# Kernel optimization log

Hardware: AMD Instinct MI355X
Metric: run time of the kernel (lower is better)

## Reference

```python
import jax, jax.numpy as jnp
import numpy as np

EMBED_DIM = 1024
NUM_HEADS = 16
HEAD_DIM = EMBED_DIM // NUM_HEADS
FEATURE_EPS = 1e-06
DEN_EPS = 1e-06


def setup_inputs() -> dict:
    key = jax.random.key(0)
    k_x, k_qw, k_qb, k_ow, k_ob = jax.random.split(key, 5)
    b, l = 2, 2048
    x = jax.random.normal(k_x, (b, l, EMBED_DIM), dtype=jnp.float32)
    s = 1.0 / np.sqrt(EMBED_DIM)
    qkv_w = jax.random.uniform(k_qw, (3 * EMBED_DIM, EMBED_DIM), minval=-s, maxval=s, dtype=jnp.float32)
    qkv_b = jax.random.uniform(k_qb, (3 * EMBED_DIM,), minval=-s, maxval=s, dtype=jnp.float32)
    out_w = jax.random.uniform(k_ow, (EMBED_DIM, EMBED_DIM), minval=-s, maxval=s, dtype=jnp.float32)
    out_b = jax.random.uniform(k_ob, (EMBED_DIM,), minval=-s, maxval=s, dtype=jnp.float32)
    return {"x": x, "qkv_w": qkv_w, "qkv_b": qkv_b, "out_w": out_w, "out_b": out_b}


def reference(x, qkv_w, qkv_b, out_w, out_b):
    b, l, e = x.shape
    # qkv projection -> (3, b, h, l, d)
    qkv = (x @ qkv_w.T + qkv_b).reshape(b, l, 3, NUM_HEADS, HEAD_DIM)
    qkv = jnp.transpose(qkv, (2, 0, 3, 1, 4))
    q, k, v = qkv[0], qkv[1], qkv[2]
    # phi(x) = relu(x) + eps
    q = jax.nn.relu(q) + FEATURE_EPS
    k = jax.nn.relu(k) + FEATURE_EPS
    # running outer-product state: (b, h, l, d, d)
    kv = jnp.cumsum(jnp.einsum('bhld,bhle->bhlde', k, v), axis=2)
    k_cum = jnp.cumsum(k, axis=2)
    num = jnp.einsum('bhld,bhlde->bhle', q, kv)
    den = jnp.maximum(jnp.einsum('bhld,bhld->bhl', q, k_cum)[..., None], DEN_EPS)
    out = num / den  # (b, h, l, d)
    out = jnp.transpose(out, (0, 2, 1, 3)).reshape(b, l, e)
    return out @ out_w.T + out_b
```

## Files before the change

kernel.cpp:

```cpp
#include <hip/hip_runtime.h>
#include <hip/hip_bf16.h>
#include <cstdint>

#define B_ 2
#define L_ 2048
#define E_ 1024
#define H_ 16
#define D_ 64
#define N3_ 3072
#define NCHUNK 32
#define CHUNK 64

typedef __attribute__((ext_vector_type(8))) short bf16x8;
typedef __attribute__((ext_vector_type(4))) float f32x4;

__device__ __forceinline__ unsigned short f2bf(float f) {
  unsigned u = __float_as_uint(f);
  unsigned r = (u + 0x7fffu + ((u >> 16) & 1u)) >> 16;
  return (unsigned short)r;
}

__global__ __launch_bounds__(256) void k_cvt_all(
    const float* __restrict__ x, const float* __restrict__ qkv_w,
    const float* __restrict__ out_w, unsigned short* __restrict__ xb,
    unsigned short* __restrict__ wqkv, unsigned short* __restrict__ wout) {
  const int i = blockIdx.x * 256 + threadIdx.x;
  const float* src;
  unsigned short* dst;
  int j;
  if (i < 1048576)      { src = x;     dst = xb;   j = i; }
  else if (i < 1835008) { src = qkv_w; dst = wqkv; j = i - 1048576; }
  else                  { src = out_w; dst = wout; j = i - 1835008; }
  float4 v = reinterpret_cast<const float4*>(src)[j];
  ushort4 o;
  o.x = f2bf(v.x); o.y = f2bf(v.y); o.z = f2bf(v.z); o.w = f2bf(v.w);
  reinterpret_cast<ushort4*>(dst)[j] = o;
}

__global__ __launch_bounds__(512, 2) void k_gemm256_qkv(
    const unsigned short* __restrict__ A,
    const unsigned short* __restrict__ Bm,
    const float* __restrict__ bias,
    unsigned short* __restrict__ Qb, unsigned short* __restrict__ Kb,
    unsigned short* __restrict__ Vb) {
  __shared__ short As[2][256 * 64];
  __shared__ short Bs[2][192 * 64];
  const int tid = threadIdx.x;
  const int lane = tid & 63, wave = tid >> 6;
  const int wm = wave >> 2, wn = wave & 3;
  const int bid0 = blockIdx.y * 16 + blockIdx.x;
  const int bid = (bid0 & 7) * 32 + (bid0 >> 3);
  const int m0 = (bid >> 4) * 256, n0 = (bid & 15) * 192;
  const int srow = tid >> 3, scol = (tid & 7) * 8;
  const int ssw = (srow & 7) * 8;
  const int l15 = lane & 15, l16 = lane >> 4;
  const int sw = (l15 & 7) * 8;
  const int NT = 16;

  f32x4 acc[8][3];
#pragma unroll
  for (int i = 0; i < 8; ++i)
#pragma unroll
    for (int j = 0; j < 3; ++j) acc[i][j] = (f32x4){0.f, 0.f, 0.f, 0.f};

  auto stageA = [&](int d, int kt) {
#pragma unroll
    for (int i = 0; i < 4; ++i) {
      const int r = i * 64 + srow;
      const unsigned short* src = &A[(size_t)(m0 + r) * 1024 + kt * 64 + (scol ^ ssw)];
      __builtin_amdgcn_global_load_lds(
          (const __attribute__((address_space(1))) unsigned int*)src,
          (__attribute__((address_space(3))) unsigned int*)&As[d][r * 64 + scol], 16, 0, 0);
    }
  };
  auto stageB = [&](int d, int kt) {
#pragma unroll
    for (int i = 0; i < 3; ++i) {
      const int r = i * 64 + srow;
      const unsigned short* src = &Bm[(size_t)(n0 + r) * 1024 + kt * 64 + (scol ^ ssw)];
      __builtin_amdgcn_global_load_lds(
          (const __attribute__((address_space(1))) unsigned int*)src,
          (__attribute__((address_space(3))) unsigned int*)&Bs[d][r * 64 + scol], 16, 0, 0);
    }
  };
  auto lda = [&](bf16x8 (&dv)[8], int d, int kh) {
#pragma unroll
    for (int mi = 0; mi < 8; ++mi) {
      const int r = wm * 128 + mi * 16 + l15;
      dv[mi] = *reinterpret_cast<const bf16x8*>(&As[d][r * 64 + ((l16 * 8 + kh * 32) ^ sw)]);
    }
  };
  auto ldb = [&](bf16x8 (&dv)[3], int d, int kh) {
#pragma unroll
    for (int ni = 0; ni < 3; ++ni) {
      const int r = wn * 48 + ni * 16 + l15;
      dv[ni] = *reinterpret_cast<const bf16x8*>(&Bs[d][r * 64 + ((l16 * 8 + kh * 32) ^ sw)]);
    }
  };
  auto quad = [&](const bf16x8 (&af)[8], const bf16x8 (&bf)[3], int nb, int ne) {
    __builtin_amdgcn_s_setprio(1);
#pragma unroll
    for (int mi = 0; mi < 8; ++mi)
      for (int nn = nb; nn < ne; ++nn)
        acc[mi][nn] = __builtin_amdgcn_mfma_f32_16x16x32_bf16(af[mi], bf[nn], acc[mi][nn], 0, 0, 0);
    __builtin_amdgcn_s_setprio(0);
  };

  stageA(0, 0); stageB(0, 0); stageA(1, 1);
  asm volatile("s_waitcnt vmcnt(4)" ::: "memory");
  __builtin_amdgcn_s_barrier();

  bf16x8 af0[8], af1[8], bf0[3], bf1[3];
  for (int t = 0; t < NT; ++t) {
    const int d = t & 1;
    lda(af0, d, 0); ldb(bf0, d, 0);
    if (t + 1 < NT) stageB(d ^ 1, t + 1);
    __builtin_amdgcn_s_barrier();
    asm volatile("s_waitcnt lgkmcnt(0)" ::: "memory");
    __builtin_amdgcn_sched_barrier(0);
    quad(af0, bf0, 0, 2);
    __builtin_amdgcn_s_barrier();
    lda(af1, d, 1); ldb(bf1, d, 1);
    __builtin_amdgcn_s_barrier();
    asm volatile("s_waitcnt lgkmcnt(0)" ::: "memory");
    __builtin_amdgcn_sched_barrier(0);
    quad(af0, bf0, 2, 3);
    __builtin_amdgcn_s_barrier();
    if (t + 2 < NT) stageA(d, t + 2);
    quad(af1, bf1, 0, 2);
    __builtin_amdgcn_s_barrier();
    quad(af1, bf1, 2, 3);
    if (t + 2 < NT) asm volatile("s_waitcnt vmcnt(4)" ::: "memory");
    else            asm volatile("s_waitcnt vmcnt(0)" ::: "memory");
    __builtin_amdgcn_s_barrier();
  }

#pragma unroll
  for (int mi = 0; mi < 8; ++mi) {
#pragma unroll
    for (int ni = 0; ni < 3; ++ni) {
      const int col = n0 + wn * 48 + ni * 16 + l15;
      const float bv = bias[col];
      const int t = col >> 10, hd = col & 1023;
      const int h = hd >> 6, dd = hd & 63;
#pragma unroll
      for (int j = 0; j < 4; ++j) {
        const int row = m0 + wm * 128 + mi * 16 + l16 * 4 + j;
        const float val = acc[mi][ni][j] + bv;
        const int b = row >> 11, l = row & 2047;
        const size_t dst = (((size_t)(b * 16 + h)) * 2048 + l) * 64 + dd;
        if (t == 0)      Qb[dst] = f2bf(fmaxf(val, 0.f) + 1e-6f);
        else if (t == 1) Kb[dst] = f2bf(fmaxf(val, 0.f) + 1e-6f);
        else             Vb[dst] = f2bf(val);
      }
    }
  }
}

__global__ __launch_bounds__(256) void k_gemm_out(
    const unsigned short* __restrict__ A, const unsigned short* __restrict__ Bm,
    const float* __restrict__ bias, float* __restrict__ O, const int K) {
  __shared__ short As[128 * 32];
  __shared__ short Bs[128 * 32];
  const int tid = threadIdx.x;
  const int lane = tid & 63;
  const int wave = tid >> 6;
  const int wr = wave >> 1, wc = wave & 1;
  const int m0 = blockIdx.y * 128, n0 = blockIdx.x * 128;
  const int srow = tid >> 2;
  const int scol = (tid & 3) << 3;
  f32x4 acc[4][4];
#pragma unroll
  for (int i = 0; i < 4; ++i)
#pragma unroll
    for (int j = 0; j < 4; ++j) acc[i][j] = (f32x4){0.f, 0.f, 0.f, 0.f};

  const int l15 = lane & 15, l16 = lane >> 4;
  const int aoff0 = (wr * 64 + l15) * 32 + l16 * 8;
  const int boff0 = (wc * 64 + l15) * 32 + l16 * 8;

  for (int k0 = 0; k0 < K; k0 += 32) {
    const short* gA = (const short*)&A[(size_t)(m0 + srow) * K + k0 + scol];
    const short* gB = (const short*)&Bm[(size_t)(n0 + srow) * K + k0 + scol];
    __builtin_amdgcn_global_load_lds(
        (const __attribute__((address_space(1))) unsigned int*)gA,
        (__attribute__((address_space(3))) unsigned int*)&As[tid * 8], 16, 0, 0);
    __builtin_amdgcn_global_load_lds(
        (const __attribute__((address_space(1))) unsigned int*)(gA + (size_t)64 * K),
        (__attribute__((address_space(3))) unsigned int*)&As[2048 + tid * 8], 16, 0, 0);
    __builtin_amdgcn_global_load_lds(
        (const __attribute__((address_space(1))) unsigned int*)gB,
        (__attribute__((address_space(3))) unsigned int*)&Bs[tid * 8], 16, 0, 0);
    __builtin_amdgcn_global_load_lds(
        (const __attribute__((address_space(1))) unsigned int*)(gB + (size_t)64 * K),
        (__attribute__((address_space(3))) unsigned int*)&Bs[2048 + tid * 8], 16, 0, 0);
    __syncthreads();
    bf16x8 af[4], bfr[4];
#pragma unroll
    for (int f = 0; f < 4; ++f)
      af[f] = *reinterpret_cast<const bf16x8*>(&As[aoff0 + f * 16 * 32]);
#pragma unroll
    for (int f = 0; f < 4; ++f)
      bfr[f] = *reinterpret_cast<const bf16x8*>(&Bs[boff0 + f * 16 * 32]);
#pragma unroll
    for (int m = 0; m < 4; ++m)
#pragma unroll
      for (int n = 0; n < 4; ++n)
        acc[m][n] = __builtin_amdgcn_mfma_f32_16x16x32_bf16(af[m], bfr[n], acc[m][n], 0, 0, 0);
    __syncthreads();
  }

  const int rbase = l16 * 4;
#pragma unroll
  for (int m = 0; m < 4; ++m) {
#pragma unroll
    for (int n = 0; n < 4; ++n) {
      const int col = n0 + wc * 64 + n * 16 + l15;
      const float bv = bias[col];
#pragma unroll
      for (int j = 0; j < 4; ++j) {
        const int row = m0 + wr * 64 + m * 16 + rbase + j;
        O[(size_t)row * 1024 + col] = acc[m][n][j] + bv;
      }
    }
  }
}

__global__ __launch_bounds__(128) void k_chunkB(
    const unsigned short* __restrict__ Kb, const unsigned short* __restrict__ Vb,
    float* __restrict__ ST, unsigned short* __restrict__ Vtb) {
  __shared__ __align__(16) unsigned short Kt[64 * 72];
  __shared__ __align__(16) unsigned short Vt[64 * 72];
  const int tid = threadIdx.x;
  const int lane = tid & 63, w = tid >> 6;
  const int c = lane & 15, g = lane >> 4;
  const int bid = blockIdx.x;
  const int bh = bid >> 5, ch = bid & 31;
  const size_t base = ((size_t)bh * L_ + (size_t)ch * CHUNK) * D_;
  const int l = tid >> 1, hf = tid & 1;
  bf16x8 kv[4], vv[4];
#pragma unroll
  for (int i = 0; i < 4; ++i) {
    kv[i] = *reinterpret_cast<const bf16x8*>(&Kb[base + (size_t)l * 64 + hf * 32 + i * 8]);
    vv[i] = *reinterpret_cast<const bf16x8*>(&Vb[base + (size_t)l * 64 + hf * 32 + i * 8]);
  }
#pragma unroll
  for (int i = 0; i < 4; ++i)
#pragma unroll
    for (int r = 0; r < 8; ++r) {
      const int d = hf * 32 + i * 8 + r;
      Kt[d * 72 + l] = (unsigned short)kv[i][r];
      Vt[d * 72 + l] = (unsigned short)vv[i][r];
    }
  __syncthreads();
  bf16x8 kf[4][2], vf[2][2];
#pragma unroll
  for (int dt = 0; dt < 4; ++dt)
#pragma unroll
    for (int kh = 0; kh < 2; ++kh)
      kf[dt][kh] = *reinterpret_cast<const bf16x8*>(&Kt[(dt * 16 + c) * 72 + g * 8 + kh * 32]);
#pragma unroll
  for (int ei = 0; ei < 2; ++ei)
#pragma unroll
    for (int kh = 0; kh < 2; ++kh)
      vf[ei][kh] = *reinterpret_cast<const bf16x8*>(&Vt[((w * 2 + ei) * 16 + c) * 72 + g * 8 + kh * 32]);
  f32x4 acc[2][4];
#pragma unroll
  for (int ei = 0; ei < 2; ++ei)
#pragma unroll
    for (int dt = 0; dt < 4; ++dt) acc[ei][dt] = (f32x4){0.f, 0.f, 0.f, 0.f};
#pragma unroll
  for (int ei = 0; ei < 2; ++ei)
#pragma unroll
    for (int dt = 0; dt < 4; ++dt)
#pragma unroll
      for (int kh = 0; kh < 2; ++kh)
        acc[ei][dt] = __builtin_amdgcn_mfma_f32_16x16x32_bf16(vf[ei][kh], kf[dt][kh], acc[ei][dt], 0, 0, 0);
  const size_t stbase = (size_t)bid * 5120;
#pragma unroll
  for (int ei = 0; ei < 2; ++ei)
#pragma unroll
    for (int dt = 0; dt < 4; ++dt)
#pragma unroll
      for (int r = 0; r < 4; ++r)
        ST[stbase + (size_t)((w * 2 + ei) * 16 + 4 * g + r) * 64 + dt * 16 + c] = acc[ei][dt][r];
#pragma unroll
  for (int ei = 0; ei < 2; ++ei)
#pragma unroll
    for (int kh = 0; kh < 2; ++kh)
      *reinterpret_cast<bf16x8*>(&Vtb[(size_t)bid * 4096 + ((w * 2 + ei) * 16 + c) * 64 + g * 8 + kh * 32]) = vf[ei][kh];
  if (w == 0) {
    const short one = (c == 0) ? (short)0x3F80 : (short)0;
    bf16x8 of;
#pragma unroll
    for (int r = 0; r < 8; ++r) of[r] = one;
    f32x4 az[4];
#pragma unroll
    for (int dt = 0; dt < 4; ++dt) az[dt] = (f32x4){0.f, 0.f, 0.f, 0.f};
#pragma unroll
    for (int dt = 0; dt < 4; ++dt)
#pragma unroll
      for (int kh = 0; kh < 2; ++kh)
        az[dt] = __builtin_amdgcn_mfma_f32_16x16x32_bf16(of, kf[dt][kh], az[dt], 0, 0, 0);
    if (g == 0) {
#pragma unroll
      for (int dt = 0; dt < 4; ++dt)
        ST[stbase + 64 * 64 + dt * 16 + c] = az[dt][0];
    }
  }
}

__global__ __launch_bounds__(256) void k_prefix2(const float* __restrict__ ST,
                                                 unsigned short* __restrict__ STb) {
  const int bh = blockIdx.x;
  const int e = blockIdx.y * 256 + threadIdx.x;
  if (e >= 4160) return;
  const size_t base = (size_t)bh * NCHUNK * 5120 + e;
  float run = 0.f;
  for (int cc = 0; cc < NCHUNK; ++cc) {
    const float t = ST[base + (size_t)cc * 5120];
    STb[base + (size_t)cc * 5120] = f2bf(run);
    run += t;
  }
}

__global__ __launch_bounds__(256) void k_chunkD(
    const unsigned short* __restrict__ Qb, const unsigned short* __restrict__ Kb,
    const unsigned short* __restrict__ Vtb, const unsigned short* __restrict__ STb,
    unsigned short* __restrict__ attnb) {
  __shared__ __align__(16) unsigned short P[4][1024];
  const int tid = threadIdx.x;
  const int lane = tid & 63, lt = tid >> 6;
  const int c = lane & 15, g = lane >> 4;
  const int bid = blockIdx.x;
  const int bh = bid >> 5, ch = bid & 31;
  const int b = bh >> 4, h = bh & 15;
  const size_t qkbase = ((size_t)bh * L_ + (size_t)ch * CHUNK) * D_;
  bf16x8 q[2], k4[4][2], s[5][2], vt[4][2], pa[2];
#pragma unroll
  for (int kh = 0; kh < 2; ++kh)
    q[kh] = *reinterpret_cast<const bf16x8*>(&Qb[qkbase + (size_t)(lt * 16 + c) * 64 + g * 8 + kh * 32]);
#pragma unroll
  for (int jt = 0; jt < 4; ++jt)
#pragma unroll
    for (int kh = 0; kh < 2; ++kh)
      k4[jt][kh] = *reinterpret_cast<const bf16x8*>(&Kb[qkbase + (size_t)(jt * 16 + c) * 64 + g * 8 + kh * 32]);
  const size_t stbase = (size_t)bid * 5120;
#pragma unroll
  for (int et = 0; et < 5; ++et)
#pragma unroll
    for (int kh = 0; kh < 2; ++kh)
      s[et][kh] = *reinterpret_cast<const bf16x8*>(&STb[stbase + (size_t)(et * 16 + c) * 64 + g * 8 + kh * 32]);
#pragma unroll
  for (int et = 0; et < 4; ++et)
#pragma unroll
    for (int kh = 0; kh < 2; ++kh)
      vt[et][kh] = *reinterpret_cast<const bf16x8*>(&Vtb[(size_t)bid * 4096 + (size_t)(et * 16 + c) * 64 + g * 8 + kh * 32]);

  char* Pb = (char*)&P[lt][0];
  const int swz = (c & 7) << 4;
#pragma unroll
  for (int jt = 0; jt < 4; ++jt) {
    unsigned pk0 = 0, pk1 = 0;
    if (jt <= lt) {
      f32x4 a1 = (f32x4){0.f, 0.f, 0.f, 0.f};
#pragma unroll
      for (int kh = 0; kh < 2; ++kh)
        a1 = __builtin_amdgcn_mfma_f32_16x16x32_bf16(k4[jt][kh], q[kh], a1, 0, 0, 0);
      if (jt == lt) {
#pragma unroll
        for (int r = 0; r < 4; ++r) a1[r] = (4 * g + r <= c) ? a1[r] : 0.f;
      }
      pk0 = (unsigned)f2bf(a1[0]) | ((unsigned)f2bf(a1[1]) << 16);
      pk1 = (unsigned)f2bf(a1[2]) | ((unsigned)f2bf(a1[3]) << 16);
    }
    *reinterpret_cast<unsigned*>(Pb + ((c * 128 + 32 * jt + 8 * g + 0) ^ swz)) = pk0;
    *reinterpret_cast<unsigned*>(Pb + ((c * 128 + 32 * jt + 8 * g + 4) ^ swz)) = pk1;
  }
#pragma unroll
  for (int kh = 0; kh < 2; ++kh)
    pa[kh] = *reinterpret_cast<const bf16x8*>(Pb + (c * 128 + ((16 * g + 64 * kh) ^ swz)));

  f32x4 acc2[5];
#pragma unroll
  for (int et = 0; et < 5; ++et) acc2[et] = (f32x4){0.f, 0.f, 0.f, 0.f};
  const short one = (c == 0) ? (short)0x3F80 : (short)0;
  bf16x8 of;
#pragma unroll
  for (int r = 0; r < 8; ++r) of[r] = one;
#pragma unroll
  for (int et = 0; et < 5; ++et) {
#pragma unroll
    for (int kh = 0; kh < 2; ++kh) {
      acc2[et] = __builtin_amdgcn_mfma_f32_16x16x32_bf16(q[kh], s[et][kh], acc2[et], 0, 0, 0);
      bf16x8 vv = (et < 4) ? vt[et][kh] : of;
      acc2[et] = __builtin_amdgcn_mfma_f32_16x16x32_bf16(pa[kh], vv, acc2[et], 0, 0, 0);
    }
  }
  float inv[4];
#pragma unroll
  for (int r = 0; r < 4; ++r) {
    float dv = __shfl(acc2[4][r], lane & 48, 64);
    inv[r] = 1.f / fmaxf(dv, 1e-6f);
  }
  const size_t obase = ((size_t)b * L_ + (size_t)ch * CHUNK + (size_t)lt * 16) * E_ + (size_t)h * 64;
#pragma unroll
  for (int et = 0; et < 4; ++et)
#pragma unroll
    for (int r = 0; r < 4; ++r)
      attnb[obase + (size_t)(4 * g + r) * E_ + et * 16 + c] = f2bf(acc2[et][r] * inv[r]);
}

extern "C" void kernel_launch(void* const* d_in, const int* in_sizes, int n_in,
                              void* d_out, int out_size, void* d_ws, size_t ws_size,
                              hipStream_t stream) {
  const float* x = (const float*)d_in[0];
  const float* qkv_w = (const float*)d_in[1];
  const float* qkv_b = (const float*)d_in[2];
  const float* out_w = (const float*)d_in[3];
  const float* out_b = (const float*)d_in[4];
  float* out = (float*)d_out;

  const size_t SZ = (size_t)B_ * H_ * L_ * D_;
  char* p = (char*)d_ws;
  unsigned short* Qb = (unsigned short*)p;    p += SZ * 2;
  unsigned short* Kb = (unsigned short*)p;    p += SZ * 2;
  unsigned short* Vb = (unsigned short*)p;    p += SZ * 2;
  unsigned short* Vtb = (unsigned short*)p;   p += (size_t)1024 * 4096 * 2;
  float* ST = (float*)p;                      p += (size_t)1024 * 5120 * 4;
  unsigned short* STb = (unsigned short*)p;   p += (size_t)1024 * 5120 * 2;
  unsigned short* xb = (unsigned short*)p;    p += SZ * 2;
  unsigned short* wqkv = (unsigned short*)p;  p += (size_t)N3_ * E_ * 2;
  unsigned short* wout = (unsigned short*)p;  p += (size_t)E_ * E_ * 2;
  unsigned short* attnb = (unsigned short*)p; p += SZ * 2;

  dim3 blk(256);
  k_cvt_all<<<dim3(8192), blk, 0, stream>>>(x, qkv_w, out_w, xb, wqkv, wout);
  k_gemm256_qkv<<<dim3(16, 16), dim3(512), 0, stream>>>(xb, wqkv, qkv_b, Qb, Kb, Vb);
  k_chunkB<<<dim3(1024), dim3(128), 0, stream>>>(Kb, Vb, ST, Vtb);
  k_prefix2<<<dim3(32, 17), blk, 0, stream>>>(ST, STb);
  k_chunkD<<<dim3(1024), blk, 0, stream>>>(Qb, Kb, Vtb, STb, attnb);
  k_gemm_out<<<dim3(E_ / 128, (B_ * L_) / 128), blk, 0, stream>>>(
      attnb, wout, out_b, out, E_);
}
```

Baseline: 173.6 us.

## Pipeline output GEMM with 256x64 double-buffered tiles and store chunk states in bf16

Replaces the single-buffered 128x128 output projection GEMM with a 512-thread kernel that uses 256x64 tiles. It double-buffers shared memory with asynchronous global-to-LDS loads, XOR-swizzles the LDS layout, remaps blocks for locality and raises wave priority around MFMA groups. The goal is to overlap loads with compute and cut LDS bank conflicts. It also stores per-chunk states in bf16 instead of fp32, halving traffic between chunkB and the prefix kernel, at the cost of extra rounding before the prefix sum.

```diff
diff --git a/kernel.cpp b/kernel.cpp
--- a/kernel.cpp
+++ b/kernel.cpp
@@ -18,6 +18,9 @@
   unsigned u = __float_as_uint(f);
   unsigned r = (u + 0x7fffu + ((u >> 16) & 1u)) >> 16;
   return (unsigned short)r;
+}
+__device__ __forceinline__ float bf2f(unsigned short u) {
+  return __uint_as_float(((unsigned)u) << 16);
 }
 
 __global__ __launch_bounds__(256) void k_cvt_all(
@@ -157,78 +160,107 @@
   }
 }
 
-__global__ __launch_bounds__(256) void k_gemm_out(
-    const unsigned short* __restrict__ A, const unsigned short* __restrict__ Bm,
-    const float* __restrict__ bias, float* __restrict__ O, const int K) {
-  __shared__ short As[128 * 32];
-  __shared__ short Bs[128 * 32];
+__global__ __launch_bounds__(512, 2) void k_gemm256_out(
+    const unsigned short* __restrict__ A,
+    const unsigned short* __restrict__ Bm,
+    const float* __restrict__ bias, float* __restrict__ O) {
+  __shared__ short As[2][256 * 64];
+  __shared__ short Bs[2][64 * 64];
   const int tid = threadIdx.x;
-  const int lane = tid & 63;
-  const int wave = tid >> 6;
-  const int wr = wave >> 1, wc = wave & 1;
-  const int m0 = blockIdx.y * 128, n0 = blockIdx.x * 128;
-  const int srow = tid >> 2;
-  const int scol = (tid & 3) << 3;
-  f32x4 acc[4][4];
-#pragma unroll
-  for (int i = 0; i < 4; ++i)
-#pragma unroll
-    for (int j = 0; j < 4; ++j) acc[i][j] = (f32x4){0.f, 0.f, 0.f, 0.f};
-
+  const int lane = tid & 63, wave = tid >> 6;
+  const int wm = wave >> 2, wn = wave & 3;
+  const int bid0 = blockIdx.y * 16 + blockIdx.x;
+  const int bid = (bid0 & 7) * 32 + (bid0 >> 3);
+  const int m0 = (bid >> 4) * 256, n0 = (bid & 15) * 64;
+  const int srow = tid >> 3, scol = (tid & 7) * 8;
+  const int ssw = (srow & 7) * 8;
   const int l15 = lane & 15, l16 = lane >> 4;
-  const int aoff0 = (wr * 64 + l15) * 32 + l16 * 8;
-  const int boff0 = (wc * 64 + l15) * 32 + l16 * 8;
-
-  for (int k0 = 0; k0 < K; k0 += 32) {
-    const short* gA = (const short*)&A[(size_t)(m0 + srow) * K + k0 + scol];
-    const short* gB = (const short*)&Bm[(size_t)(n0 + srow) * K + k0 + scol];
+  const int sw = (l15 & 7) * 8;
+  const int NT = 16;
+
+  f32x4 acc[8];
+#pragma unroll
+  for (int i = 0; i < 8; ++i) acc[i] = (f32x4){0.f, 0.f, 0.f, 0.f};
+
+  auto stageA = [&](int d, int kt) {
+#pragma unroll
+    for (int i = 0; i < 4; ++i) {
+      const int r = i * 64 + srow;
+      const unsigned short* src = &A[(size_t)(m0 + r) * 1024 + kt * 64 + (scol ^ ssw)];
+      __builtin_amdgcn_global_load_lds(
+          (const __attribute__((address_space(1))) unsigned int*)src,
+          (__attribute__((address_space(3))) unsigned int*)&As[d][r * 64 + scol], 16, 0, 0);
+    }
+  };
+  auto stageB = [&](int d, int kt) {
+    const unsigned short* src = &Bm[(size_t)(n0 + srow) * 1024 + kt * 64 + (scol ^ ssw)];
     __builtin_amdgcn_global_load_lds(
-        (const __attribute__((address_space(1))) unsigned int*)gA,
-        (__attribute__((address_space(3))) unsigned int*)&As[tid * 8], 16, 0, 0);
-    __builtin_amdgcn_global_load_lds(
-        (const __attribute__((address_space(1))) unsigned int*)(gA + (size_t)64 * K),
-        (__attribute__((address_space(3))) unsigned int*)&As[2048 + tid * 8], 16, 0, 0);
-    __builtin_amdgcn_global_load_lds(
-        (const __attribute__((address_space(1))) unsigned int*)gB,
-        (__attribute__((address_space(3))) unsigned int*)&Bs[tid * 8], 16, 0, 0);
-    __builtin_amdgcn_global_load_lds(
-        (const __attribute__((address_space(1))) unsigned int*)(gB + (size_t)64 * K),
-        (__attribute__((address_space(3))) unsigned int*)&Bs[2048 + tid * 8], 16, 0, 0);
-    __syncthreads();
-    bf16x8 af[4], bfr[4];
-#pragma unroll
-    for (int f = 0; f < 4; ++f)
-      af[f] = *reinterpret_cast<const bf16x8*>(&As[aoff0 + f * 16 * 32]);
-#pragma unroll
-    for (int f = 0; f < 4; ++f)
-      bfr[f] = *reinterpret_cast<const bf16x8*>(&Bs[boff0 + f * 16 * 32]);
-#pragma unroll
-    for (int m = 0; m < 4; ++m)
-#pragma unroll
-      for (int n = 0; n < 4; ++n)
-        acc[m][n] = __builtin_amdgcn_mfma_f32_16x16x32_bf16(af[m], bfr[n], acc[m][n], 0, 0, 0);
-    __syncthreads();
-  }
-
-  const int rbase = l16 * 4;
-#pragma unroll
-  for (int m = 0; m < 4; ++m) {
-#pragma unroll
-    for (int n = 0; n < 4; ++n) {
-      const int col = n0 + wc * 64 + n * 16 + l15;
-      const float bv = bias[col];
-#pragma unroll
-      for (int j = 0; j < 4; ++j) {
-        const int row = m0 + wr * 64 + m * 16 + rbase + j;
-        O[(size_t)row * 1024 + col] = acc[m][n][j] + bv;
-      }
+        (const __attribute__((address_space(1))) unsigned int*)src,
+        (__attribute__((address_space(3))) unsigned int*)&Bs[d][srow * 64 + scol], 16, 0, 0);
+  };
+  auto lda = [&](bf16x8 (&dv)[8], int d, int kh) {
+#pragma unroll
+    for (int mi = 0; mi < 8; ++mi) {
+      const int r = wm * 128 + mi * 16 + l15;
+      dv[mi] = *reinterpret_cast<const bf16x8*>(&As[d][r * 64 + ((l16 * 8 + kh * 32) ^ sw)]);
+    }
+  };
+  auto ldb = [&](bf16x8& dv, int d, int kh) {
+    const int r = wn * 16 + l15;
+    dv = *reinterpret_cast<const bf16x8*>(&Bs[d][r * 64 + ((l16 * 8 + kh * 32) ^ sw)]);
+  };
+  auto half = [&](const bf16x8 (&af)[8], const bf16x8& bf, int mb) {
+    __builtin_amdgcn_s_setprio(1);
+#pragma unroll
+    for (int mi = mb; mi < mb + 4; ++mi)
+      acc[mi] = __builtin_amdgcn_mfma_f32_16x16x32_bf16(af[mi], bf, acc[mi], 0, 0, 0);
+    __builtin_amdgcn_s_setprio(0);
+  };
+
+  stageA(0, 0); stageB(0, 0); stageA(1, 1);
+  asm volatile("s_waitcnt vmcnt(4)" ::: "memory");
+  __builtin_amdgcn_s_barrier();
+
+  bf16x8 af0[8], af1[8], bf0, bf1;
+  for (int t = 0; t < NT; ++t) {
+    const int d = t & 1;
+    lda(af0, d, 0); ldb(bf0, d, 0);
+    if (t + 1 < NT) stageB(d ^ 1, t + 1);
+    __builtin_amdgcn_s_barrier();
+    asm volatile("s_waitcnt lgkmcnt(0)" ::: "memory");
+    __builtin_amdgcn_sched_barrier(0);
+    half(af0, bf0, 0);
+    __builtin_amdgcn_s_barrier();
+    lda(af1, d, 1); ldb(bf1, d, 1);
+    __builtin_amdgcn_s_barrier();
+    asm volatile("s_waitcnt lgkmcnt(0)" ::: "memory");
+    __builtin_amdgcn_sched_barrier(0);
+    half(af0, bf0, 4);
+    __builtin_amdgcn_s_barrier();
+    if (t + 2 < NT) stageA(d, t + 2);
+    half(af1, bf1, 0);
+    __builtin_amdgcn_s_barrier();
+    half(af1, bf1, 4);
+    if (t + 2 < NT) asm volatile("s_waitcnt vmcnt(4)" ::: "memory");
+    else            asm volatile("s_waitcnt vmcnt(0)" ::: "memory");
+    __builtin_amdgcn_s_barrier();
+  }
+
+  const int col = n0 + wn * 16 + l15;
+  const float bv = bias[col];
+#pragma unroll
+  for (int mi = 0; mi < 8; ++mi) {
+#pragma unroll
+    for (int j = 0; j < 4; ++j) {
+      const int row = m0 + wm * 128 + mi * 16 + l16 * 4 + j;
+      O[(size_t)row * 1024 + col] = acc[mi][j] + bv;
     }
   }
 }
 
 __global__ __launch_bounds__(128) void k_chunkB(
     const unsigned short* __restrict__ Kb, const unsigned short* __restrict__ Vb,
-    float* __restrict__ ST, unsigned short* __restrict__ Vtb) {
+    unsigned short* __restrict__ STc, unsigned short* __restrict__ Vtb) {
   __shared__ __align__(16) unsigned short Kt[64 * 72];
   __shared__ __align__(16) unsigned short Vt[64 * 72];
   const int tid = threadIdx.x;
@@ -283,7 +315,7 @@
     for (int dt = 0; dt < 4; ++dt)
 #pragma unroll
       for (int r = 0; r < 4; ++r)
-        ST[stbase + (size_t)((w * 2 + ei) * 16 + 4 * g + r) * 64 + dt * 16 + c] = acc[ei][dt][r];
+        STc[stbase + (size_t)((w * 2 + ei) * 16 + 4 * g + r) * 64 + dt * 16 + c] = f2bf(acc[ei][dt][r]);
 #pragma unroll
   for (int ei = 0; ei < 2; ++ei)
 #pragma unroll
@@ -305,12 +337,12 @@
     if (g == 0) {
 #pragma unroll
       for (int dt = 0; dt < 4; ++dt)
-        ST[stbase + 64 * 64 + dt * 16 + c] = az[dt][0];
-    }
-  }
-}
-
-__global__ __launch_bounds__(256) void k_prefix2(const float* __restrict__ ST,
+        STc[stbase + 64 * 64 + dt * 16 + c] = f2bf(az[dt][0]);
+    }
+  }
+}
+
+__global__ __launch_bounds__(256) void k_prefix2(const unsigned short* __restrict__ STc,
                                                  unsigned short* __restrict__ STb) {
   const int bh = blockIdx.x;
   const int e = blockIdx.y * 256 + threadIdx.x;
@@ -318,7 +350,7 @@
   const size_t base = (size_t)bh * NCHUNK * 5120 + e;
   float run = 0.f;
   for (int cc = 0; cc < NCHUNK; ++cc) {
-    const float t = ST[base + (size_t)cc * 5120];
+    const float t = bf2f(STc[base + (size_t)cc * 5120]);
     STb[base + (size_t)cc * 5120] = f2bf(run);
     run += t;
   }
@@ -427,7 +459,7 @@
   unsigned short* Kb = (unsigned short*)p;    p += SZ * 2;
   unsigned short* Vb = (unsigned short*)p;    p += SZ * 2;
   unsigned short* Vtb = (unsigned short*)p;   p += (size_t)1024 * 4096 * 2;
-  float* ST = (float*)p;                      p += (size_t)1024 * 5120 * 4;
+  unsigned short* STc = (unsigned short*)p;   p += (size_t)1024 * 5120 * 2;
   unsigned short* STb = (unsigned short*)p;   p += (size_t)1024 * 5120 * 2;
   unsigned short* xb = (unsigned short*)p;    p += SZ * 2;
   unsigned short* wqkv = (unsigned short*)p;  p += (size_t)N3_ * E_ * 2;
@@ -437,9 +469,8 @@
   dim3 blk(256);
   k_cvt_all<<<dim3(8192), blk, 0, stream>>>(x, qkv_w, out_w, xb, wqkv, wout);
   k_gemm256_qkv<<<dim3(16, 16), dim3(512), 0, stream>>>(xb, wqkv, qkv_b, Qb, Kb, Vb);
-  k_chunkB<<<dim3(1024), dim3(128), 0, stream>>>(Kb, Vb, ST, Vtb);
-  k_prefix2<<<dim3(32, 17), blk, 0, stream>>>(ST, STb);
+  k_chunkB<<<dim3(1024), dim3(128), 0, stream>>>(Kb, Vb, STc, Vtb);
+  k_prefix2<<<dim3(32, 17), blk, 0, stream>>>(STc, STb);
   k_chunkD<<<dim3(1024), blk, 0, stream>>>(Qb, Kb, Vtb, STb, attnb);
-  k_gemm_out<<<dim3(E_ / 128, (B_ * L_) / 128), blk, 0, stream>>>(
-      attnb, wout, out_b, out, E_);
-}
+  k_gemm256_out<<<dim3(16, 16), dim3(512), 0, stream>>>(attnb, wout, out_b, out);
+}
```

New measurement: 163.6 us. 1.06x faster.
